# Optimization experiments

Measured on AMD Instinct MI355X. Metric: run time of the kernel, lower is better.

## Reference

```python
import jax, jax.numpy as jnp
import numpy as np

B, T = 8, 256
IDIM = 80; ODIM = 80; HDIM = 256; CDIM = 64
TEMPER = 1.0; ETH = 40.0
N_ITER = HDIM // CDIM  # 4


def shift_windows(key, pad, window):
    # key: (B,T,D) -> all shifted windows (B,T,S,window), S = D + 2*pad - window + 1
    D = key.shape[-1]
    kp = jnp.pad(key, ((0, 0), (0, 0), (pad, pad)))
    S = D + 2 * pad - window + 1
    idx = jnp.arange(S)[:, None] + jnp.arange(window)[None, :]
    return kp[..., idx]


def sim_argmax(x_aug, y):
    # cosine similarity over feature dim, argmax over shift dim S
    num = jnp.einsum('btsw,btw->bts', x_aug, y)
    den = jnp.sqrt(jnp.sum(x_aug ** 2, -1)) * jnp.sqrt(jnp.sum(y ** 2, -1))[..., None] + 1e-6
    sim = num / den
    theta = jnp.argmax(sim, -1)  # (B,T)
    y_al = jnp.take_along_axis(x_aug, theta[..., None, None], 2)[..., 0, :]
    s_opt = jnp.take_along_axis(sim, theta[..., None], -1)[..., 0]
    return y_al, s_opt, theta


def reverse_shift(y_al, pad, window, theta, D):
    # place aligned window back at its original offset (inverse of shift theta)
    yp = jnp.pad(y_al, ((0, 0), (0, 0), (pad, pad)))
    S = window + 2 * pad - D + 1
    idx = jnp.arange(S)[:, None] + jnp.arange(D)[None, :]
    win = yp[..., idx]  # (B,T,S,D)
    start = 2 * pad - theta
    return jnp.take_along_axis(win, start[..., None, None], 2)[..., 0, :]


def attention(x, y, temper):
    return jax.nn.softmax(x * y / temper, axis=-1)


def seq_loss(pred, tgt, mask):
    # elementwise MSE, zeroed at padded positions (mask True)
    return jnp.where(mask, 0.0, (pred - tgt) ** 2)


def hsr(h, mask_prev, seq_mask_t):
    # topk energy masking with cross-iteration exclusivity (hidden-space regularization)
    idx = jax.lax.top_k(h ** 2, CDIM)[1]
    mask_cur = jax.nn.one_hot(idx, HDIM, dtype=h.dtype).sum(-2)
    if mask_prev is None:
        mask_new, loss_h = mask_cur, None
    else:
        inter = mask_prev * mask_cur
        lh = jnp.where(seq_mask_t[..., None], 0.0, (h - (1.0 - inter)) ** 2)
        loss_h = jnp.sum(jnp.where(inter > 0, lh, 0.0))
        h = jnp.where(mask_prev > 0, 0.0, h)
        idx = jax.lax.top_k(h ** 2, CDIM)[1]
        mask_cur = jax.nn.one_hot(idx, HDIM, dtype=h.dtype).sum(-2)
        mask_new = mask_prev + mask_cur
    return h * mask_cur, mask_new, loss_h


def conv1d_encode(z, W, b, D):
    # windowed encoder: all D+1 offsets of a width-2D window, pick max-energy offset
    zw = shift_windows(z, D, 2 * D)                 # (B,T,D+1,2D)
    h = jnp.einsum('btsw,wh->btsh', zw, W) + b      # (B,T,D+1,H)
    ind = jnp.argmax(jnp.sum(h ** 2, -1), -1)       # (B,T)
    h_sel = jnp.take_along_axis(h, ind[..., None, None], 2)[..., 0, :]
    return h_sel, ind


def conv1d_decode(h, W, b, ind, D):
    # gather length-D slice starting at the encoder's chosen offset
    ext = jnp.einsum('bth,hw->btw', h, W) + b       # (B,T,2D)
    idx = ind[..., None] + jnp.arange(D)            # (B,T,D)
    return jnp.take_along_axis(ext, idx, -1)


def _forward(x, y, We, be, Wd, bd, Wds, bds):
    seq_mask = (y == 0.0)                 # ignore_out = 0.0
    seq_mask_t = jnp.all(seq_mask, -1)    # per-timestep padding flag
    y_res, x_res = y, x
    mp_src = mp_self = None
    losses = []
    for _ in range(N_ITER):
        x_aug = shift_windows(x_res, ODIM - 1, ODIM)
        y_al, s_opt, theta = sim_argmax(x_aug, y_res)
        attn = attention(y_al, y_res, TEMPER)
        x_ele = reverse_shift(y_al * attn, ODIM - 1, ODIM, theta, IDIM)
        # self branch (conv1d)
        h_self, ind_self = conv1d_encode(x_ele, We, be, IDIM)
        h_self, mp_self, lh_self = hsr(h_self, mp_self, seq_mask_t)
        x_ele = conv1d_decode(h_self, Wds, bds, ind_self, IDIM)
        move = jnp.abs(theta - IDIM + 1)[..., None]
        ll_self = jnp.where(move > ETH, 0.0, seq_loss(x_ele, x_res, seq_mask)) / (move.astype(x.dtype) + 1.0)
        # re-align decoded x_ele to y_res
        x_aug = shift_windows(x_ele, ODIM - 1, ODIM)
        y_al, s_opt, theta = sim_argmax(x_aug, y_res)
        # src branch (conv1d)
        h_src, ind_src = conv1d_encode(y_al, We, be, IDIM)
        h_src, mp_src, lh_src = hsr(h_src, mp_src, seq_mask_t)
        y_ele = conv1d_decode(h_src, Wd, bd, ind_src, ODIM)
        move = jnp.abs(theta - ODIM + 1)[..., None]
        ll_src = jnp.where(move > ETH, 0.0, seq_loss(y_ele, y_res, seq_mask)) / (move.astype(x.dtype) + 1.0)
        loss_it = ll_src.sum() + ll_self.sum()
        if lh_src is not None:
            loss_it = loss_it + lh_src + lh_self
        losses.append(loss_it)
        y_res = jax.lax.stop_gradient(y_res - y_ele)
        x_res = jax.lax.stop_gradient(x_res - x_ele)
    return jnp.mean(jnp.stack(losses))


def setup_inputs() -> dict:
    key = jax.random.key(0)
    ks = jax.random.split(key, 8)
    return {
        'x': jax.random.normal(ks[0], (B, T, IDIM), jnp.float32),
        'y': jax.random.normal(ks[1], (B, T, ODIM), jnp.float32),
        'We': jax.random.normal(ks[2], (2 * IDIM, HDIM), jnp.float32) * 0.05,
        'be': jnp.zeros((HDIM,), jnp.float32),
        'Wd': jax.random.normal(ks[3], (HDIM, 2 * ODIM), jnp.float32) * 0.05,
        'bd': jnp.zeros((2 * ODIM,), jnp.float32),
        'Wds': jax.random.normal(ks[4], (HDIM, 2 * IDIM), jnp.float32) * 0.05,
        'bds': jnp.zeros((2 * IDIM,), jnp.float32),
    }


def reference(x, y, We, be, Wd, bd, Wds, bds):
    return _forward(x, y, We, be, Wd, bd, Wds, bds)
```

## Files before the change

### kernel.cpp

```cpp
#include <hip/hip_runtime.h>
#include <math.h>

#define NBT 2048

typedef __attribute__((ext_vector_type(8))) short short8;
typedef __attribute__((ext_vector_type(4))) float floatx4;

struct SM {
  alignas(16) float xp[240];
  alignas(16) short xhr[8][264];
  alignas(16) short xlr[8][264];
  alignas(16) unsigned hkey[256];
  alignas(16) float yres[80];
  alignas(16) float beL[256];
  alignas(16) float spad[240];
  alignas(16) int2  dpair[64];
  alignas(16) float energyP[4][96];
  float xres[80];
  float yal[80];
  float xele[80];
  float decsrc[80];
  float zb[80];
  float energy[96];
  unsigned char mp_self[256];
  unsigned char mp_src[256];
  float ext[160];
  unsigned char smask[80];
  int smask_t;
  float abv[4];
  int   abi[4];
  int   wcnt[4];
  float nys;
};

__device__ __forceinline__ float waveSum(float v){
  #pragma unroll
  for (int off = 32; off > 0; off >>= 1) v += __shfl_xor(v, off, 64);
  return v;
}
__device__ __forceinline__ int waveSumI(int v){
  #pragma unroll
  for (int off = 32; off > 0; off >>= 1) v += __shfl_xor(v, off, 64);
  return v;
}
__device__ __forceinline__ float waveMax(float v){
  #pragma unroll
  for (int off = 32; off > 0; off >>= 1) v = fmaxf(v, __shfl_xor(v, off, 64));
  return v;
}

__device__ __forceinline__ int blockArgMax(SM& sm, float v, int idx){
  int lane = threadIdx.x & 63, w = threadIdx.x >> 6;
  #pragma unroll
  for (int off = 32; off > 0; off >>= 1){
    float ov = __shfl_xor(v,   off, 64);
    int   oi = __shfl_xor(idx, off, 64);
    if (ov > v || (ov == v && oi < idx)){ v = ov; idx = oi; }
  }
  if (lane == 0){ sm.abv[w] = v; sm.abi[w] = idx; }
  __syncthreads();
  float bv = sm.abv[0]; int bi = sm.abi[0];
  #pragma unroll
  for (int w2 = 1; w2 < 4; w2++){
    float ov = sm.abv[w2]; int oi = sm.abi[w2];
    if (ov > bv || (ov == bv && oi < bi)){ bv = ov; bi = oi; }
  }
  __syncthreads();
  return bi;
}

__device__ __forceinline__ int rankTop64(SM& sm, unsigned myb, int tid, int w){
  int cnt = 0;
  const uint4* q4 = (const uint4*)sm.hkey;
  int b0 = 16 * w, b1 = b0 + 16;
  #pragma unroll 4
  for (int i4 = 0; i4 < b0; i4++){
    uint4 o = q4[i4];
    cnt += (o.x >= myb) ? 1 : 0;
    cnt += (o.y >= myb) ? 1 : 0;
    cnt += (o.z >= myb) ? 1 : 0;
    cnt += (o.w >= myb) ? 1 : 0;
  }
  #pragma unroll 4
  for (int i4 = b0; i4 < b1; i4++){
    uint4 o = q4[i4];
    int i = 4 * i4;
    cnt += ((o.x > myb) || (o.x == myb && (i    ) < tid)) ? 1 : 0;
    cnt += ((o.y > myb) || (o.y == myb && (i + 1) < tid)) ? 1 : 0;
    cnt += ((o.z > myb) || (o.z == myb && (i + 2) < tid)) ? 1 : 0;
    cnt += ((o.w > myb) || (o.w == myb && (i + 3) < tid)) ? 1 : 0;
  }
  #pragma unroll 4
  for (int i4 = b1; i4 < 64; i4++){
    uint4 o = q4[i4];
    cnt += (o.x > myb) ? 1 : 0;
    cnt += (o.y > myb) ? 1 : 0;
    cnt += (o.z > myb) ? 1 : 0;
    cnt += (o.w > myb) ? 1 : 0;
  }
  return (cnt < 64) ? 1 : 0;
}

__device__ __forceinline__ void compactSel(SM& sm, int sel, float val){
  int tid = threadIdx.x, lane = tid & 63, w = tid >> 6;
  unsigned long long mq = __ballot(sel != 0);
  if (lane == 0) sm.wcnt[w] = __popcll(mq);
  __syncthreads();
  int base = 0;
  #pragma unroll
  for (int i = 0; i < 4; i++) base += (i < w) ? sm.wcnt[i] : 0;
  if (sel){
    unsigned long long below = (lane == 0) ? 0ull : ((~0ull) >> (64 - lane));
    int pos = base + (int)__popcll(mq & below);
    sm.dpair[pos] = make_int2(tid, __float_as_int(val));
  }
  __syncthreads();
}

__device__ __forceinline__ int simArgmax(SM& sm, const float* src, float* yal_out, int doNy){
  int tid = threadIdx.x;
  int lane = tid & 63, w = tid >> 6;
  __syncthreads();
  if (tid < 240) sm.spad[tid] = (tid >= 79 && tid < 159) ? src[tid - 79] : 0.f;
  if (doNy && w == 0){
    float yv2 = 0.f;
    for (int i = lane; i < 80; i += 64){ float yv = sm.yres[i]; yv2 = fmaf(yv, yv, yv2); }
    float ny = sqrtf(waveSum(yv2));
    if (lane == 0) sm.nys = ny;
  }
  __syncthreads();
  float nys = sm.nys;
  float bv = -INFINITY; int bi = 0;
  if (tid < 159){
    const float4* y4p = (const float4*)sm.yres;
    float num = 0.f, nx = 0.f;
    for (int w4 = 0; w4 < 20; w4++){
      float4 yy = y4p[w4];
      int wb = w4 * 4;
      float xa0 = sm.spad[tid + wb + 0];
      float xa1 = sm.spad[tid + wb + 1];
      float xa2 = sm.spad[tid + wb + 2];
      float xa3 = sm.spad[tid + wb + 3];
      num = fmaf(xa0, yy.x, num); nx = fmaf(xa0, xa0, nx);
      num = fmaf(xa1, yy.y, num); nx = fmaf(xa1, xa1, nx);
      num = fmaf(xa2, yy.z, num); nx = fmaf(xa2, xa2, nx);
      num = fmaf(xa3, yy.w, num); nx = fmaf(xa3, xa3, nx);
    }
    bv = num / (sqrtf(nx) * nys + 1e-6f);
    bi = tid;
  }
  int th = blockArgMax(sm, bv, bi);
  if (tid < 80) yal_out[tid] = sm.spad[th + tid];
  __syncthreads();
  return th;
}

template<int USE_WS>
__device__ __forceinline__ void branchCompute(
    SM& sm, const float* __restrict__ We,
    const short8* __restrict__ wsB,
    const float* __restrict__ Wdec, const float* __restrict__ bdec,
    const float* enc_in, unsigned char* mask, const float* target,
    float* dec_out, int theta, bool first, float& lossAcc)
{
  int tid = threadIdx.x;
  int lane = tid & 63, w = tid >> 6;
  int quad = lane >> 4, l15 = lane & 15;
  __syncthreads();
  {
    float v = (tid >= 80 && tid < 160) ? enc_in[tid - 80] : 0.f;
    if (tid < 240) sm.xp[tid] = v;
    unsigned bits = __float_as_uint(v);
    unsigned hi = bits >> 16;
    float hif = __uint_as_float(hi << 16);
    unsigned lo = __float_as_uint(v - hif) >> 16;
    short hs = (short)hi, ls = (short)lo;
    #pragma unroll
    for (int c = 0; c < 8; c++){
      int i = tid - c;
      if (i >= 0){ sm.xhr[c][i] = hs; sm.xlr[c][i] = ls; }
    }
  }
  __syncthreads();

  const floatx4 zero4 = {0.f, 0.f, 0.f, 0.f};
  const int ng = w;
  const int c8 = l15 & 7;
  const int hb = l15 >> 3;

  #pragma unroll 1
  for (int mt = 0; mt < 6; mt++){
    const int ktlo = (mt == 0) ? 2 : ((mt <= 2) ? 1 : 0);
    const int kthi = (mt <= 1) ? 5 : ((mt <= 3) ? 4 : 3);
    floatx4 acc[4];
    #pragma unroll
    for (int nt = 0; nt < 4; nt++) acc[nt] = zero4;

    #pragma unroll 1
    for (int kt = ktlo; kt < kthi; kt++){
      int kb = quad + 2 * mt + 4 * kt + hb;
      short8 Ah = *reinterpret_cast<const short8*>(&sm.xhr[c8][8 * kb]);
      short8 Al = *reinterpret_cast<const short8*>(&sm.xlr[c8][8 * kb]);
      #pragma unroll 1
      for (int nt = 0; nt < 4; nt++){
        short8 Bh, Bl;
        int tileIdx = kt * 16 + (ng * 4 + nt);
        if (USE_WS){
          int ti2 = (tileIdx * 64 + lane) * 2;
          Bh = wsB[ti2];
          Bl = wsB[ti2 + 1];
        } else {
          short8 bh, bl;
          int k0 = kt * 32 + quad * 8;
          int n  = (ng * 4 + nt) * 16 + l15;
          #pragma unroll
          for (int j = 0; j < 8; j++){
            float v = We[(k0 + j) * 256 + n];
            unsigned bits = __float_as_uint(v);
            unsigned hi = bits >> 16;
            float hif = __uint_as_float(hi << 16);
            unsigned lo = __float_as_uint(v - hif) >> 16;
            bh[j] = (short)hi; bl[j] = (short)lo;
          }
          Bh = bh; Bl = bl;
        }
        acc[nt] = __builtin_amdgcn_mfma_f32_16x16x32_bf16(Ah, Bh, acc[nt], 0, 0, 0);
        acc[nt] = __builtin_amdgcn_mfma_f32_16x16x32_bf16(Al, Bh, acc[nt], 0, 0, 0);
        acc[nt] = __builtin_amdgcn_mfma_f32_16x16x32_bf16(Ah, Bl, acc[nt], 0, 0, 0);
      }
    }

    float bn[4];
    #pragma unroll
    for (int nt = 0; nt < 4; nt++) bn[nt] = sm.beL[(ng * 4 + nt) * 16 + l15];
    float er[4];
    #pragma unroll
    for (int r = 0; r < 4; r++){
      float s_ = 0.f;
      #pragma unroll
      for (int nt = 0; nt < 4; nt++){
        float hvv = acc[nt][r] + bn[nt];
        s_ = fmaf(hvv, hvv, s_);
      }
      er[r] = s_;
    }
    #pragma unroll
    for (int x2 = 1; x2 < 16; x2 <<= 1){
      #pragma unroll
      for (int r = 0; r < 4; r++) er[r] += __shfl_xor(er[r], x2, 64);
    }
    if (l15 == 0){
      #pragma unroll
      for (int r = 0; r < 4; r++)
        sm.energyP[w][mt * 16 + quad * 4 + r] = er[r];
    }
  }
  __syncthreads();
  if (tid < 96){
    float e = sm.energyP[0][tid];
    e += sm.energyP[1][tid];
    e += sm.energyP[2][tid];
    e += sm.energyP[3][tid];
    sm.energy[tid] = e;
  }
  __syncthreads();

  float bvE = (tid < 81) ? sm.energy[tid] : -INFINITY;
  int   biE = (tid < 81) ? tid : 0;
  int ind = blockArgMax(sm, bvE, biE);

  int roff = 80 - ind;
  float hv = sm.beL[tid];
  #pragma unroll 8
  for (int w2 = 0; w2 < 80; w2++){
    float xv = sm.xp[80 + w2];
    hv = fmaf(xv, We[(w2 + roff) * 256 + tid], hv);
  }

  float vsq = hv * hv;
  unsigned myb = __float_as_uint(vsq);
  sm.hkey[tid] = myb;
  __syncthreads();
  int sel1 = rankTop64(sm, myb, tid, w);
  unsigned char mpv = mask[tid];
  if (first){
    mask[tid] = (unsigned char)sel1;
    compactSel(sm, sel1, hv);
  } else {
    int st = sm.smask_t;
    float interv = (float)mpv * (float)sel1;
    if (interv > 0.f && !st){
      float dd = hv - (1.f - interv);
      lossAcc += dd * dd;
    }
    float h2 = (mpv > 0) ? 0.f : hv;
    __syncthreads();
    unsigned myb2 = __float_as_uint(h2 * h2);
    sm.hkey[tid] = myb2;
    __syncthreads();
    int sel2 = rankTop64(sm, myb2, tid, w);
    mask[tid] = (unsigned char)(mpv + (unsigned char)sel2);
    compactSel(sm, sel2, h2);
  }

  if (tid < 160){
    float a = bdec[tid];
    #pragma unroll 8
    for (int i = 0; i < 64; i++){
      int2 p = sm.dpair[i];
      a = fmaf(__int_as_float(p.y), Wdec[p.x * 160 + tid], a);
    }
    sm.ext[tid] = a;
  }
  __syncthreads();

  float mv = fabsf((float)(theta - 79));
  bool gate = (mv > 40.0f);
  if (tid < 80){
    float dec = sm.ext[ind + tid];
    dec_out[tid] = dec;
    float diff = dec - target[tid];
    float l = (gate || sm.smask[tid]) ? 0.f : diff * diff;
    lossAcc += l / (mv + 1.0f);
  }
  __syncthreads();
}

__global__ void __launch_bounds__(64) zero_out_kernel(float* out){
  if (threadIdx.x == 0) out[0] = 0.f;
}

__global__ void __launch_bounds__(64) prep_we_kernel(
    const float* __restrict__ We, short8* __restrict__ wsB){
  int tile = blockIdx.x;
  int lane = threadIdx.x;
  int kt = tile >> 4, nt = tile & 15;
  int k0 = kt * 32 + (lane >> 4) * 8;
  int n  = nt * 16 + (lane & 15);
  short8 h, l;
  #pragma unroll
  for (int j = 0; j < 8; j++){
    float v = We[(k0 + j) * 256 + n];
    unsigned bits = __float_as_uint(v);
    unsigned hi = bits >> 16;
    float hif = __uint_as_float(hi << 16);
    unsigned lo = __float_as_uint(v - hif) >> 16;
    h[j] = (short)hi; l[j] = (short)lo;
  }
  int ti2 = (tile * 64 + lane) * 2;
  wsB[ti2]     = h;
  wsB[ti2 + 1] = l;
}

template<int USE_WS>
__global__ void __launch_bounds__(256, 8) net_kernel(
    const float* __restrict__ x,  const float* __restrict__ y,
    const float* __restrict__ We, const float* __restrict__ be,
    const float* __restrict__ Wd, const float* __restrict__ bd,
    const float* __restrict__ Wds,const float* __restrict__ bds,
    const short8* __restrict__ wsB,
    float* out)
{
  __shared__ SM sm;
  int tid = threadIdx.x;
  int lane = tid & 63, w = tid >> 6;
  int bt  = blockIdx.x;
  const float* xin = x + bt * 80;
  const float* yin = y + bt * 80;

  if (tid < 80){
    sm.xres[tid] = xin[tid];
    float yv = yin[tid];
    sm.yres[tid] = yv;
    sm.smask[tid] = (yv == 0.f) ? 1 : 0;
  }
  sm.mp_self[tid] = 0;
  sm.mp_src[tid]  = 0;
  sm.beL[tid] = be[tid];
  __syncthreads();
  if (w == 0){
    int c = 0;
    for (int i = lane; i < 80; i += 64) c += (int)sm.smask[i];
    int total = waveSumI(c);
    if (lane == 0) sm.smask_t = (total == 80) ? 1 : 0;
  }
  __syncthreads();

  float lossAcc = 0.f;

  for (int it = 0; it < 4; it++){
    bool first = (it == 0);

    int th1 = simArgmax(sm, sm.xres, sm.yal, 1);

    if (w == 0){
      float p0 = sm.yal[lane] * sm.yres[lane];
      float p1 = (lane < 16) ? sm.yal[64 + lane] * sm.yres[64 + lane] : -INFINITY;
      float mx = waveMax(fmaxf(p0, p1));
      float e0 = expf(p0 - mx);
      float e1 = (lane < 16) ? expf(p1 - mx) : 0.f;
      float ssum = waveSum(e0 + e1);
      sm.zb[lane] = sm.yal[lane] * (e0 / ssum);
      if (lane < 16) sm.zb[64 + lane] = sm.yal[64 + lane] * (e1 / ssum);
    }
    __syncthreads();

    if (tid < 80){
      int q = tid + 79 - th1;
      sm.xele[tid] = (q >= 0 && q < 80) ? sm.zb[q] : 0.f;
    }

    branchCompute<USE_WS>(sm, We, wsB, Wds, bds,
                          sm.xele, sm.mp_self, sm.xres, sm.xele, th1, first, lossAcc);

    int th2 = simArgmax(sm, sm.xele, sm.yal, 0);

    branchCompute<USE_WS>(sm, We, wsB, Wd, bd,
                          sm.yal, sm.mp_src, sm.yres, sm.decsrc, th2, first, lossAcc);

    __syncthreads();
    if (tid < 80){
      sm.xres[tid] -= sm.xele[tid];
      sm.yres[tid] -= sm.decsrc[tid];
    }
    __syncthreads();
  }

  float vsum = waveSum(lossAcc);
  if (lane == 0) sm.abv[w] = vsum;
  __syncthreads();
  if (tid == 0){
    float total = ((sm.abv[0] + sm.abv[1]) + sm.abv[2]) + sm.abv[3];
    atomicAdd(out, total * 0.25f);
  }
}

extern "C" void kernel_launch(void* const* d_in, const int* in_sizes, int n_in,
                              void* d_out, int out_size, void* d_ws, size_t ws_size,
                              hipStream_t stream) {
  const float* x   = (const float*)d_in[0];
  const float* y   = (const float*)d_in[1];
  const float* We  = (const float*)d_in[2];
  const float* be  = (const float*)d_in[3];
  const float* Wd  = (const float*)d_in[4];
  const float* bd  = (const float*)d_in[5];
  const float* Wds = (const float*)d_in[6];
  const float* bds = (const float*)d_in[7];
  float* out = (float*)d_out;

  const size_t fragCount = 80 * 64 * 2;
  const size_t fragBytes = fragCount * sizeof(short8);
  int use_ws = (ws_size >= fragBytes) ? 1 : 0;
  short8* wsB = (short8*)d_ws;

  hipLaunchKernelGGL(zero_out_kernel, dim3(1), dim3(64), 0, stream, out);
  if (use_ws){
    hipLaunchKernelGGL(prep_we_kernel, dim3(80), dim3(64), 0, stream, We, wsB);
    hipLaunchKernelGGL((net_kernel<1>), dim3(NBT), dim3(256), 0, stream,
                       x, y, We, be, Wd, bd, Wds, bds, wsB, out);
  } else {
    hipLaunchKernelGGL((net_kernel<0>), dim3(NBT), dim3(256), 0, stream,
                       x, y, We, be, Wd, bd, Wds, bds, wsB, out);
  }
}
```

Before: 678.7 us.

## Process two M-tiles per K step to reuse B fragments across MFMAs

Restructures the energy MFMA loop so each iteration handles two M-tiles together, loading each B (We hi/lo) fragment once and using it for both tiles. This halves the global/workspace B loads and gives more independent MFMAs to interleave. The K-range per tile pair is widened to cover both tiles' ranges, so some zero-region MFMAs may be computed redundantly. Launch bounds are relaxed from 8 to 4 blocks per SM to allow more registers for the doubled accumulators, which can reduce occupancy.

```diff
diff --git a/kernel.cpp b/kernel.cpp
--- a/kernel.cpp
+++ b/kernel.cpp
@@ -189,19 +189,26 @@
   const int hb = l15 >> 3;
 
   #pragma unroll 1
-  for (int mt = 0; mt < 6; mt++){
-    const int ktlo = (mt == 0) ? 2 : ((mt <= 2) ? 1 : 0);
-    const int kthi = (mt <= 1) ? 5 : ((mt <= 3) ? 4 : 3);
-    floatx4 acc[4];
+  for (int mh = 0; mh < 3; mh++){
+    int ktlo = (mh == 0) ? 1 : 0;
+    int kthi = 5 - mh;
+    floatx4 acc[2][4];
     #pragma unroll
-    for (int nt = 0; nt < 4; nt++) acc[nt] = zero4;
+    for (int m2 = 0; m2 < 2; m2++)
+      #pragma unroll
+      for (int nt = 0; nt < 4; nt++) acc[m2][nt] = zero4;
 
     #pragma unroll 1
     for (int kt = ktlo; kt < kthi; kt++){
-      int kb = quad + 2 * mt + 4 * kt + hb;
-      short8 Ah = *reinterpret_cast<const short8*>(&sm.xhr[c8][8 * kb]);
-      short8 Al = *reinterpret_cast<const short8*>(&sm.xlr[c8][8 * kb]);
-      #pragma unroll 1
+      short8 Ah[2], Al[2];
+      #pragma unroll
+      for (int m2 = 0; m2 < 2; m2++){
+        int mt = mh * 2 + m2;
+        int kb = quad + 2 * mt + 4 * kt + hb;
+        Ah[m2] = *reinterpret_cast<const short8*>(&sm.xhr[c8][8 * kb]);
+        Al[m2] = *reinterpret_cast<const short8*>(&sm.xlr[c8][8 * kb]);
+      }
+      #pragma unroll 2
       for (int nt = 0; nt < 4; nt++){
         short8 Bh, Bl;
         int tileIdx = kt * 16 + (ng * 4 + nt);
@@ -224,35 +231,42 @@
           }
           Bh = bh; Bl = bl;
         }
-        acc[nt] = __builtin_amdgcn_mfma_f32_16x16x32_bf16(Ah, Bh, acc[nt], 0, 0, 0);
-        acc[nt] = __builtin_amdgcn_mfma_f32_16x16x32_bf16(Al, Bh, acc[nt], 0, 0, 0);
-        acc[nt] = __builtin_amdgcn_mfma_f32_16x16x32_bf16(Ah, Bl, acc[nt], 0, 0, 0);
+        acc[0][nt] = __builtin_amdgcn_mfma_f32_16x16x32_bf16(Ah[0], Bh, acc[0][nt], 0, 0, 0);
+        acc[0][nt] = __builtin_amdgcn_mfma_f32_16x16x32_bf16(Al[0], Bh, acc[0][nt], 0, 0, 0);
+        acc[0][nt] = __builtin_amdgcn_mfma_f32_16x16x32_bf16(Ah[0], Bl, acc[0][nt], 0, 0, 0);
+        acc[1][nt] = __builtin_amdgcn_mfma_f32_16x16x32_bf16(Ah[1], Bh, acc[1][nt], 0, 0, 0);
+        acc[1][nt] = __builtin_amdgcn_mfma_f32_16x16x32_bf16(Al[1], Bh, acc[1][nt], 0, 0, 0);
+        acc[1][nt] = __builtin_amdgcn_mfma_f32_16x16x32_bf16(Ah[1], Bl, acc[1][nt], 0, 0, 0);
       }
     }
 
     float bn[4];
     #pragma unroll
     for (int nt = 0; nt < 4; nt++) bn[nt] = sm.beL[(ng * 4 + nt) * 16 + l15];
-    float er[4];
     #pragma unroll
-    for (int r = 0; r < 4; r++){
-      float s_ = 0.f;
+    for (int m2 = 0; m2 < 2; m2++){
+      int mt = mh * 2 + m2;
+      float er[4];
       #pragma unroll
-      for (int nt = 0; nt < 4; nt++){
-        float hvv = acc[nt][r] + bn[nt];
-        s_ = fmaf(hvv, hvv, s_);
+      for (int r = 0; r < 4; r++){
+        float s_ = 0.f;
+        #pragma unroll
+        for (int nt = 0; nt < 4; nt++){
+          float hvv = acc[m2][nt][r] + bn[nt];
+          s_ = fmaf(hvv, hvv, s_);
+        }
+        er[r] = s_;
       }
-      er[r] = s_;
-    }
-    #pragma unroll
-    for (int x2 = 1; x2 < 16; x2 <<= 1){
       #pragma unroll
-      for (int r = 0; r < 4; r++) er[r] += __shfl_xor(er[r], x2, 64);
-    }
-    if (l15 == 0){
-      #pragma unroll
-      for (int r = 0; r < 4; r++)
-        sm.energyP[w][mt * 16 + quad * 4 + r] = er[r];
+      for (int x2 = 1; x2 < 16; x2 <<= 1){
+        #pragma unroll
+        for (int r = 0; r < 4; r++) er[r] += __shfl_xor(er[r], x2, 64);
+      }
+      if (l15 == 0){
+        #pragma unroll
+        for (int r = 0; r < 4; r++)
+          sm.energyP[w][mt * 16 + quad * 4 + r] = er[r];
+      }
     }
   }
   __syncthreads();
@@ -353,7 +367,7 @@
 }
 
 template<int USE_WS>
-__global__ void __launch_bounds__(256, 8) net_kernel(
+__global__ void __launch_bounds__(256, 4) net_kernel(
     const float* __restrict__ x,  const float* __restrict__ y,
     const float* __restrict__ We, const float* __restrict__ be,
     const float* __restrict__ Wd, const float* __restrict__ bd,
```

Measured after the change: 669.2 us. Within noise of the previous version (-1.4%).
